# Kernel optimization log

Hardware: AMD Instinct MI355X
Metric: run time of the kernel (lower is better)

Reference implementation:

```python
import jax, jax.numpy as jnp
import numpy as np

B, S, HID = 16, 512, 2048
H = 4
D = HID // H  # 512; module requires S == D
SCALE = 1.0 / np.sqrt(D).astype(np.float32)


def setup_inputs() -> dict:
    key = jax.random.key(0)
    ks = jax.random.split(key, 6)
    std = 0.02
    inp = {"hidden_states": jax.random.normal(ks[0], (B, S, HID), jnp.float32)}
    names = ["q", "k", "v", "ck", "cv"]
    for i, n in enumerate(names):
        inp[f"W{n}"] = jax.random.normal(ks[i + 1], (HID, HID), jnp.float32) * std
        inp[f"b{n}"] = jnp.zeros((HID,), jnp.float32)
    return inp


def _heads(x):
    # [B,S,HID] -> [B,H,S,D]
    return x.reshape(B, S, H, D).transpose(0, 2, 1, 3)


def reference(hidden_states, Wq, bq, Wk, bk, Wv, bv, Wck, bck, Wcv, bcv):
    q = _heads(hidden_states @ Wq.T + bq)
    k = _heads(hidden_states @ Wk.T + bk)
    v = _heads(hidden_states @ Wv.T + bv)
    ck = _heads(hidden_states @ Wck.T + bck)
    cv = _heads(hidden_states @ Wcv.T + bcv)

    # scores1[b,h,q,j] = sum_d Q[b,h,q,d] K[b,h,j,d]
    s1 = jnp.einsum('bhqd,bhjd->bhqj', q, k)
    # scores2 = scores1 @ cube_key^T (valid since S == D)
    s2 = jnp.einsum('bhqj,bhmj->bhqm', s1, ck) * SCALE
    probs = jax.nn.softmax(s2, axis=-1)
    # ctx1 = probs @ V : [B,H,S,D]
    ctx = jnp.einsum('bhqm,bhmd->bhqd', probs, v)
    # ctx2 = ctx1 @ cube_value : [S,D]@[S,D] valid since S == D
    ctx = jnp.einsum('bhqm,bhme->bhqe', ctx, cv)
    # merge heads: [B,H,S,D] -> [B,S,HID]
    return ctx.transpose(0, 2, 1, 3).reshape(B, S, HID)
```

## Files before the change

### kernel.cpp

```cpp
#include <hip/hip_runtime.h>
#include <math.h>


typedef _Float16 f16;
typedef f16 f16x8 __attribute__((ext_vector_type(8)));
typedef float f32x4 __attribute__((ext_vector_type(4)));
typedef float f32x16 __attribute__((ext_vector_type(16)));

#define SB_STRIDE 520
#define QBLK 128
#define CHAIN_LDS (QBLK * SB_STRIDE * 2)
#define PROJ_LDS  131072

static constexpr float SCALE = 0.04419417382415922f;

__device__ __forceinline__ void gl_lds16(const f16* g, f16* l)
{
    __builtin_amdgcn_global_load_lds(
        (const __attribute__((address_space(1))) void*)g,
        (__attribute__((address_space(3))) void*)l, 16, 0, 0);
}

__global__ __launch_bounds__(256) void conv_f32_f16(const float* __restrict__ src,
                                                    f16* __restrict__ dst, int n)
{
    int i = (blockIdx.x * 256 + threadIdx.x) * 8;
    if (i + 8 <= n) {
        float4 a = *(const float4*)(src + i);
        float4 b = *(const float4*)(src + i + 4);
        f16 o[8] = {(f16)a.x, (f16)a.y, (f16)a.z, (f16)a.w,
                    (f16)b.x, (f16)b.y, (f16)b.z, (f16)b.w};
        *(int4*)(dst + i) = *(int4*)o;
    }
}

struct ProjPtrs {
    const f16* W[5];
    const float* bias[5];
    f16* dst[5];
};

__global__ __launch_bounds__(512, 2) void proj_f16(const f16* __restrict__ A, ProjPtrs P)
{
    extern __shared__ f16 sm[];
    const int z = blockIdx.z;
    const f16* __restrict__ W = P.W[z];
    const float* __restrict__ bias = P.bias[z];
    f16* __restrict__ dst = P.dst[z];
    const bool tr = (z == 2) || (z == 4);

    const int t    = threadIdx.x;
    const int lane = t & 63;
    const int wave = t >> 6;
    const int wr   = wave >> 2, wc = wave & 3;
    const int bm = blockIdx.y * 256, bn = blockIdx.x * 256;
    const int r16 = lane & 15;
    const int kq  = lane >> 4;

    const f16* gA = A + (size_t)(bm + (wave >> 1) * 16 + r16) * 2048 + ((wave & 1) * 4 + kq) * 8;
    const f16* gB = W + (size_t)(bn + (wave >> 1) * 16 + r16) * 2048 + ((wave & 1) * 4 + kq) * 8;
    const int stoff = wave * 512;

#define STG_A(c, h, tt)                                                     \
    {                                                                       \
        f16* d_ = sm + (c) * 32768 + (h) * 8192 + stoff;                    \
        gl_lds16(gA + (size_t)((h) * 128) * 2048 + (tt) * 64, d_);          \
        gl_lds16(gA + (size_t)((h) * 128 + 64) * 2048 + (tt) * 64, d_ + 4096); \
    }
#define STG_B(c, h, tt)                                                     \
    {                                                                       \
        f16* d_ = sm + (c) * 32768 + 16384 + (h) * 8192 + stoff;            \
        gl_lds16(gB + (size_t)((h) * 128) * 2048 + (tt) * 64, d_);          \
        gl_lds16(gB + (size_t)((h) * 128 + 64) * 2048 + (tt) * 64, d_ + 4096); \
    }

    f32x4 acc[8][4];
#pragma unroll
    for (int mf = 0; mf < 8; ++mf)
#pragma unroll
        for (int nf = 0; nf < 4; ++nf)
#pragma unroll
            for (int r = 0; r < 4; ++r) acc[mf][nf][r] = 0.f;

    STG_A(0, 0, 0); STG_A(0, 1, 0); STG_B(0, 0, 0); STG_B(0, 1, 0);
    STG_A(1, 0, 1); STG_A(1, 1, 1);
    asm volatile("s_waitcnt vmcnt(4)" ::: "memory");
    __builtin_amdgcn_s_barrier();
    asm volatile("" ::: "memory");

    const int aoff = kq * 128 + r16 * 8;

    f16x8 af[8][2], bf[4][2];

    for (int kt = 0; kt < 32; ++kt) {
        const int cur = kt & 1, nxt = cur ^ 1;
        const f16* pa = sm + cur * 32768 + wr * 8192 + aoff;
        const f16* pb = sm + cur * 32768 + 16384 + (wc >> 1) * 8192 + (wc & 1) * 4096 + aoff;

#pragma unroll
        for (int mf = 0; mf < 4; ++mf)
#pragma unroll
            for (int dk = 0; dk < 2; ++dk)
                af[mf][dk] = *(const f16x8*)(pa + mf * 1024 + dk * 512);
#pragma unroll
        for (int nf = 0; nf < 2; ++nf)
#pragma unroll
            for (int dk = 0; dk < 2; ++dk)
                bf[nf][dk] = *(const f16x8*)(pb + nf * 1024 + dk * 512);
        if (kt + 1 < 32) STG_B(nxt, 0, kt + 1);
        asm volatile("" ::: "memory");
        __builtin_amdgcn_s_barrier();
        asm volatile("s_waitcnt lgkmcnt(0)" ::: "memory");
        __builtin_amdgcn_sched_barrier(0);
        __builtin_amdgcn_s_setprio(1);
#pragma unroll
        for (int mf = 0; mf < 4; ++mf)
#pragma unroll
            for (int nf = 0; nf < 2; ++nf)
#pragma unroll
                for (int dk = 0; dk < 2; ++dk)
                    acc[mf][nf] = __builtin_amdgcn_mfma_f32_16x16x32_f16(
                        af[mf][dk], bf[nf][dk], acc[mf][nf], 0, 0, 0);
        __builtin_amdgcn_s_setprio(0);
        asm volatile("" ::: "memory");
        __builtin_amdgcn_s_barrier();
        asm volatile("" ::: "memory");

#pragma unroll
        for (int mf = 4; mf < 8; ++mf)
#pragma unroll
            for (int dk = 0; dk < 2; ++dk)
                af[mf][dk] = *(const f16x8*)(pa + mf * 1024 + dk * 512);
        if (kt + 1 < 32) STG_B(nxt, 1, kt + 1);
        asm volatile("" ::: "memory");
        __builtin_amdgcn_s_barrier();
        asm volatile("s_waitcnt lgkmcnt(0)" ::: "memory");
        __builtin_amdgcn_sched_barrier(0);
        __builtin_amdgcn_s_setprio(1);
#pragma unroll
        for (int mf = 4; mf < 8; ++mf)
#pragma unroll
            for (int nf = 0; nf < 2; ++nf)
#pragma unroll
                for (int dk = 0; dk < 2; ++dk)
                    acc[mf][nf] = __builtin_amdgcn_mfma_f32_16x16x32_f16(
                        af[mf][dk], bf[nf][dk], acc[mf][nf], 0, 0, 0);
        __builtin_amdgcn_s_setprio(0);
        asm volatile("" ::: "memory");
        __builtin_amdgcn_s_barrier();
        asm volatile("" ::: "memory");

#pragma unroll
        for (int nf = 2; nf < 4; ++nf)
#pragma unroll
            for (int dk = 0; dk < 2; ++dk)
                bf[nf][dk] = *(const f16x8*)(pb + nf * 1024 + dk * 512);
        if (kt + 2 < 32) STG_A(cur, 0, kt + 2);
        asm volatile("" ::: "memory");
        __builtin_amdgcn_s_barrier();
        asm volatile("s_waitcnt lgkmcnt(0)" ::: "memory");
        __builtin_amdgcn_sched_barrier(0);
        __builtin_amdgcn_s_setprio(1);
#pragma unroll
        for (int mf = 0; mf < 4; ++mf)
#pragma unroll
            for (int nf = 2; nf < 4; ++nf)
#pragma unroll
                for (int dk = 0; dk < 2; ++dk)
                    acc[mf][nf] = __builtin_amdgcn_mfma_f32_16x16x32_f16(
                        af[mf][dk], bf[nf][dk], acc[mf][nf], 0, 0, 0);
        __builtin_amdgcn_s_setprio(0);
        asm volatile("" ::: "memory");
        __builtin_amdgcn_s_barrier();
        asm volatile("" ::: "memory");

        if (kt + 2 < 32) STG_A(cur, 1, kt + 2);
        if (kt < 30) asm volatile("s_waitcnt vmcnt(4)" ::: "memory");
        else         asm volatile("s_waitcnt vmcnt(0)" ::: "memory");
        __builtin_amdgcn_s_barrier();
        asm volatile("" ::: "memory");
        __builtin_amdgcn_s_setprio(1);
#pragma unroll
        for (int mf = 4; mf < 8; ++mf)
#pragma unroll
            for (int nf = 2; nf < 4; ++nf)
#pragma unroll
                for (int dk = 0; dk < 2; ++dk)
                    acc[mf][nf] = __builtin_amdgcn_mfma_f32_16x16x32_f16(
                        af[mf][dk], bf[nf][dk], acc[mf][nf], 0, 0, 0);
        __builtin_amdgcn_s_setprio(0);
        asm volatile("" ::: "memory");
        __builtin_amdgcn_s_barrier();
        asm volatile("" ::: "memory");
    }
#undef STG_A
#undef STG_B

    const int wm = wr * 128, wn = wc * 64;
#pragma unroll
    for (int nf = 0; nf < 4; ++nf) {
        int n = bn + wn + nf * 16 + r16;
        float bb = bias[n];
        int h = n >> 9, d = n & 511;
#pragma unroll
        for (int mf = 0; mf < 8; ++mf) {
            int mbase = bm + wm + mf * 16 + (lane >> 4) * 4;
            int b = mbase >> 9, s0 = mbase & 511;
            if (!tr) {
#pragma unroll
                for (int r = 0; r < 4; ++r)
                    dst[(((size_t)(b * 4 + h)) * 512 + s0 + r) * 512 + d] =
                        (f16)(acc[mf][nf][r] + bb);
            } else {
                f16 pk[4];
#pragma unroll
                for (int r = 0; r < 4; ++r) pk[r] = (f16)(acc[mf][nf][r] + bb);
                *(float2*)(dst + (((size_t)(b * 4 + h)) * 512 + d) * 512 + s0) =
                    *(float2*)pk;
            }
        }
    }
}

__device__ __forceinline__ void stage_ntr(const f16* __restrict__ Bsrc,
                                          const f16* __restrict__ Sb,
                                          int t, f32x16 acc[4][2])
{
    const int lane = t & 63;
    const int wave = t >> 6;
    const int l31  = lane & 31;
    const int l5   = (lane >> 5) * 8;

#pragma unroll
    for (int mt = 0; mt < 4; ++mt)
#pragma unroll
        for (int nt = 0; nt < 2; ++nt)
#pragma unroll
            for (int r = 0; r < 16; ++r) acc[mt][nt][r] = 0.f;

    const f16* b0 = Bsrc + (size_t)(wave * 64 + l31) * 512 + l5;
    const f16* b1 = Bsrc + (size_t)(wave * 64 + 32 + l31) * 512 + l5;

    f16x8 bfA[2][2], bfB[2][2];

#define LDP(S, pp)                                              \
    do {                                                        \
        S[0][0] = *(const f16x8*)(b0 + (pp) * 32);              \
        S[0][1] = *(const f16x8*)(b0 + (pp) * 32 + 16);         \
        S[1][0] = *(const f16x8*)(b1 + (pp) * 32);              \
        S[1][1] = *(const f16x8*)(b1 + (pp) * 32 + 16);         \
    } while (0)

    LDP(bfA, 0);
    LDP(bfB, 1);

#pragma unroll
    for (int p = 0; p < 16; ++p) {
        f16x8 (&S)[2][2] = (p & 1) ? bfB : bfA;
#pragma unroll
        for (int dkh = 0; dkh < 2; ++dkh) {
            f16x8 af0 = *(const f16x8*)(Sb + (size_t)l31 * SB_STRIDE + p * 32 + dkh * 16 + l5);
            f16x8 af1 = *(const f16x8*)(Sb + (size_t)(32 + l31) * SB_STRIDE + p * 32 + dkh * 16 + l5);
            f16x8 af2 = *(const f16x8*)(Sb + (size_t)(64 + l31) * SB_STRIDE + p * 32 + dkh * 16 + l5);
            f16x8 af3 = *(const f16x8*)(Sb + (size_t)(96 + l31) * SB_STRIDE + p * 32 + dkh * 16 + l5);
            acc[0][0] = __builtin_amdgcn_mfma_f32_32x32x16_f16(af0, S[0][dkh], acc[0][0], 0, 0, 0);
            acc[0][1] = __builtin_amdgcn_mfma_f32_32x32x16_f16(af0, S[1][dkh], acc[0][1], 0, 0, 0);
            acc[1][0] = __builtin_amdgcn_mfma_f32_32x32x16_f16(af1, S[0][dkh], acc[1][0], 0, 0, 0);
            acc[1][1] = __builtin_amdgcn_mfma_f32_32x32x16_f16(af1, S[1][dkh], acc[1][1], 0, 0, 0);
            acc[2][0] = __builtin_amdgcn_mfma_f32_32x32x16_f16(af2, S[0][dkh], acc[2][0], 0, 0, 0);
            acc[2][1] = __builtin_amdgcn_mfma_f32_32x32x16_f16(af2, S[1][dkh], acc[2][1], 0, 0, 0);
            acc[3][0] = __builtin_amdgcn_mfma_f32_32x32x16_f16(af3, S[0][dkh], acc[3][0], 0, 0, 0);
            acc[3][1] = __builtin_amdgcn_mfma_f32_32x32x16_f16(af3, S[1][dkh], acc[3][1], 0, 0, 0);
        }
        if (p + 2 < 16) LDP(S, p + 2);
    }
#undef LDP
}

__device__ __forceinline__ void emit_to_S(f16* __restrict__ Sb, const f32x16 acc[4][2],
                                          int t, float scale)
{
    const int lane = t & 63;
    const int wn = (t >> 6) * 64;
#pragma unroll
    for (int mt = 0; mt < 4; ++mt)
#pragma unroll
        for (int nt = 0; nt < 2; ++nt) {
            int col = wn + nt * 32 + (lane & 31);
#pragma unroll
            for (int r = 0; r < 16; ++r) {
                int row = mt * 32 + (r & 3) + 8 * (r >> 2) + 4 * (lane >> 5);
                Sb[(size_t)row * SB_STRIDE + col] = (f16)(acc[mt][nt][r] * scale);
            }
        }
}

__global__ __launch_bounds__(512, 2) void chain_f16(
    const f16* __restrict__ q16, const f16* __restrict__ k16,
    const f16* __restrict__ ck16, const f16* __restrict__ vt16,
    const f16* __restrict__ cvt16, float* __restrict__ out,
    int bhmask, int q0shift)
{
    extern __shared__ f16 smem[];
    f16* Sb = smem;
    const int t = threadIdx.x;
    const int bh = blockIdx.x & bhmask;
    const int q0 = (blockIdx.x >> q0shift) * QBLK;
    const size_t SB = 512 * 512;

    const f16* Q = q16 + bh * SB;
    for (int i = t; i < 8192; i += 512) {
        int row = i >> 6, c = (i & 63) * 8;
        *(int4*)(Sb + (size_t)row * SB_STRIDE + c) =
            *(const int4*)(Q + (size_t)(q0 + row) * 512 + c);
    }
    __syncthreads();

    f32x16 acc[4][2];

    stage_ntr(k16 + bh * SB, Sb, t, acc);
    __syncthreads();
    emit_to_S(Sb, acc, t, 1.0f);
    __syncthreads();

    stage_ntr(ck16 + bh * SB, Sb, t, acc);
    __syncthreads();
    emit_to_S(Sb, acc, t, SCALE);
    __syncthreads();

    {
        const int lane = t & 63;
        const int wave = t >> 6;
        for (int rr = 0; rr < 16; ++rr) {
            int r = wave * 16 + rr;
            f16x8 xv = *(const f16x8*)(Sb + (size_t)r * SB_STRIDE + lane * 8);
            float x[8];
            float mx = -1e30f;
#pragma unroll
            for (int j = 0; j < 8; ++j) { x[j] = (float)xv[j]; mx = fmaxf(mx, x[j]); }
#pragma unroll
            for (int o = 32; o > 0; o >>= 1) mx = fmaxf(mx, __shfl_xor(mx, o));
            float s = 0.f;
#pragma unroll
            for (int j = 0; j < 8; ++j) { x[j] = __expf(x[j] - mx); s += x[j]; }
#pragma unroll
            for (int o = 32; o > 0; o >>= 1) s += __shfl_xor(s, o);
            float inv = 1.0f / s;
            f16x8 ov;
#pragma unroll
            for (int j = 0; j < 8; ++j) ov[j] = (f16)(x[j] * inv);
            *(f16x8*)(Sb + (size_t)r * SB_STRIDE + lane * 8) = ov;
        }
    }
    __syncthreads();

    stage_ntr(vt16 + bh * SB, Sb, t, acc);
    __syncthreads();
    emit_to_S(Sb, acc, t, 1.0f);
    __syncthreads();

    stage_ntr(cvt16 + bh * SB, Sb, t, acc);
    {
        const int lane = t & 63;
        const int wn = (t >> 6) * 64;
        int b = bh >> 2, h = bh & 3;
#pragma unroll
        for (int mt = 0; mt < 4; ++mt)
#pragma unroll
            for (int nt = 0; nt < 2; ++nt) {
                int col = h * 512 + wn + nt * 32 + (lane & 31);
#pragma unroll
                for (int r = 0; r < 16; ++r) {
                    int row = q0 + mt * 32 + (r & 3) + 8 * (r >> 2) + 4 * (lane >> 5);
                    out[((size_t)b * 512 + row) * 2048 + col] = acc[mt][nt][r];
                }
            }
    }
}

extern "C" void kernel_launch(void* const* d_in, const int* in_sizes, int n_in,
                              void* d_out, int out_size, void* d_ws, size_t ws_size,
                              hipStream_t stream)
{
    const float* hs = (const float*)d_in[0];
    const float* Wf[5] = {(const float*)d_in[1], (const float*)d_in[3],
                          (const float*)d_in[5], (const float*)d_in[7],
                          (const float*)d_in[9]};
    const float* bf[5] = {(const float*)d_in[2], (const float*)d_in[4],
                          (const float*)d_in[6], (const float*)d_in[8],
                          (const float*)d_in[10]};
    float* out = (float*)d_out;

    hipFuncSetAttribute((const void*)chain_f16,
                        hipFuncAttributeMaxDynamicSharedMemorySize, CHAIN_LDS);
    hipFuncSetAttribute((const void*)proj_f16,
                        hipFuncAttributeMaxDynamicSharedMemorySize, PROJ_LDS);

    f16* ws = (f16*)d_ws;
    const size_t WELEM = 2048ULL * 2048;
    const size_t FULLACT = 64ULL * 512 * 512;

    f16* W16[5];
    for (int i = 0; i < 5; ++i) W16[i] = ws + i * WELEM;
    f16* after_w = ws + 5 * WELEM;

    for (int i = 0; i < 5; ++i)
        conv_f32_f16<<<dim3(WELEM / 2048), 256, 0, stream>>>(Wf[i], W16[i], (int)WELEM);

    size_t full_need = (5 * WELEM + FULLACT + 5 * FULLACT) * sizeof(f16);
    if (ws_size >= full_need) {
        f16* hs16 = after_w;
        f16* act[5];
        for (int i = 0; i < 5; ++i) act[i] = after_w + FULLACT + i * FULLACT;

        conv_f32_f16<<<dim3(FULLACT / 2048), 256, 0, stream>>>(hs, hs16, (int)FULLACT);

        ProjPtrs P;
        for (int i = 0; i < 5; ++i) { P.W[i] = W16[i]; P.bias[i] = bf[i]; P.dst[i] = act[i]; }
        proj_f16<<<dim3(8, 32, 5), 512, PROJ_LDS, stream>>>(hs16, P);

        chain_f16<<<dim3(256), 512, CHAIN_LDS, stream>>>(
            act[0], act[1], act[3], act[2], act[4], out, 63, 6);
    } else {
        const size_t CHROW = 1048576ULL;
        const size_t CHACT = 4ULL * 512 * 512;
        f16* hs16c = after_w;
        f16* act[5];
        for (int i = 0; i < 5; ++i) act[i] = after_w + CHROW + i * CHACT;

        ProjPtrs P;
        for (int i = 0; i < 5; ++i) { P.W[i] = W16[i]; P.bias[i] = bf[i]; P.dst[i] = act[i]; }

        for (int c = 0; c < 16; ++c) {
            conv_f32_f16<<<dim3(CHROW / 2048), 256, 0, stream>>>(
                hs + c * CHROW, hs16c, (int)CHROW);
            proj_f16<<<dim3(8, 2, 5), 512, PROJ_LDS, stream>>>(hs16c, P);
            chain_f16<<<dim3(16), 512, CHAIN_LDS, stream>>>(
                act[0], act[1], act[3], act[2], act[4], out + c * CHROW, 3, 2);
        }
    }

    (void)in_sizes; (void)n_in; (void)out_size;
}
```

Baseline: 663.6 us.

## Double chain kernel to 16 waves with half the per-wave tile; swap proj grid order

The chain kernel now runs 1024 threads (16 waves), each computing a 128x32 output slice instead of 128x64. That halves the accumulator registers and B-fragment loads per wave and doubles the waves available to hide LDS and global latency. The softmax loop and Q staging are adjusted to match. Separately, the projection grid swaps the x/y block mapping so consecutive blocks walk the M dimension, which changes L2 reuse of weight tiles. The cost is that each A fragment read from LDS now feeds two fewer MFMAs per wave, raising total LDS traffic.

```diff
diff --git a/kernel.cpp b/kernel.cpp
--- a/kernel.cpp
+++ b/kernel.cpp
@@ -53,7 +53,7 @@
     const int lane = t & 63;
     const int wave = t >> 6;
     const int wr   = wave >> 2, wc = wave & 3;
-    const int bm = blockIdx.y * 256, bn = blockIdx.x * 256;
+    const int bm = blockIdx.x * 256, bn = blockIdx.y * 256;
     const int r16 = lane & 15;
     const int kq  = lane >> 4;
 
@@ -224,7 +224,7 @@
 
 __device__ __forceinline__ void stage_ntr(const f16* __restrict__ Bsrc,
                                           const f16* __restrict__ Sb,
-                                          int t, f32x16 acc[4][2])
+                                          int t, f32x16 acc[4])
 {
     const int lane = t & 63;
     const int wave = t >> 6;
@@ -234,21 +234,16 @@
 #pragma unroll
     for (int mt = 0; mt < 4; ++mt)
 #pragma unroll
-        for (int nt = 0; nt < 2; ++nt)
-#pragma unroll
-            for (int r = 0; r < 16; ++r) acc[mt][nt][r] = 0.f;
-
-    const f16* b0 = Bsrc + (size_t)(wave * 64 + l31) * 512 + l5;
-    const f16* b1 = Bsrc + (size_t)(wave * 64 + 32 + l31) * 512 + l5;
-
-    f16x8 bfA[2][2], bfB[2][2];
+        for (int r = 0; r < 16; ++r) acc[mt][r] = 0.f;
+
+    const f16* b0 = Bsrc + (size_t)(wave * 32 + l31) * 512 + l5;
+
+    f16x8 bfA[2], bfB[2];
 
 #define LDP(S, pp)                                              \
     do {                                                        \
-        S[0][0] = *(const f16x8*)(b0 + (pp) * 32);              \
-        S[0][1] = *(const f16x8*)(b0 + (pp) * 32 + 16);         \
-        S[1][0] = *(const f16x8*)(b1 + (pp) * 32);              \
-        S[1][1] = *(const f16x8*)(b1 + (pp) * 32 + 16);         \
+        S[0] = *(const f16x8*)(b0 + (pp) * 32);                 \
+        S[1] = *(const f16x8*)(b0 + (pp) * 32 + 16);            \
     } while (0)
 
     LDP(bfA, 0);
@@ -256,46 +251,40 @@
 
 #pragma unroll
     for (int p = 0; p < 16; ++p) {
-        f16x8 (&S)[2][2] = (p & 1) ? bfB : bfA;
+        f16x8 (&S)[2] = (p & 1) ? bfB : bfA;
 #pragma unroll
         for (int dkh = 0; dkh < 2; ++dkh) {
             f16x8 af0 = *(const f16x8*)(Sb + (size_t)l31 * SB_STRIDE + p * 32 + dkh * 16 + l5);
             f16x8 af1 = *(const f16x8*)(Sb + (size_t)(32 + l31) * SB_STRIDE + p * 32 + dkh * 16 + l5);
             f16x8 af2 = *(const f16x8*)(Sb + (size_t)(64 + l31) * SB_STRIDE + p * 32 + dkh * 16 + l5);
             f16x8 af3 = *(const f16x8*)(Sb + (size_t)(96 + l31) * SB_STRIDE + p * 32 + dkh * 16 + l5);
-            acc[0][0] = __builtin_amdgcn_mfma_f32_32x32x16_f16(af0, S[0][dkh], acc[0][0], 0, 0, 0);
-            acc[0][1] = __builtin_amdgcn_mfma_f32_32x32x16_f16(af0, S[1][dkh], acc[0][1], 0, 0, 0);
-            acc[1][0] = __builtin_amdgcn_mfma_f32_32x32x16_f16(af1, S[0][dkh], acc[1][0], 0, 0, 0);
-            acc[1][1] = __builtin_amdgcn_mfma_f32_32x32x16_f16(af1, S[1][dkh], acc[1][1], 0, 0, 0);
-            acc[2][0] = __builtin_amdgcn_mfma_f32_32x32x16_f16(af2, S[0][dkh], acc[2][0], 0, 0, 0);
-            acc[2][1] = __builtin_amdgcn_mfma_f32_32x32x16_f16(af2, S[1][dkh], acc[2][1], 0, 0, 0);
-            acc[3][0] = __builtin_amdgcn_mfma_f32_32x32x16_f16(af3, S[0][dkh], acc[3][0], 0, 0, 0);
-            acc[3][1] = __builtin_amdgcn_mfma_f32_32x32x16_f16(af3, S[1][dkh], acc[3][1], 0, 0, 0);
+            acc[0] = __builtin_amdgcn_mfma_f32_32x32x16_f16(af0, S[dkh], acc[0], 0, 0, 0);
+            acc[1] = __builtin_amdgcn_mfma_f32_32x32x16_f16(af1, S[dkh], acc[1], 0, 0, 0);
+            acc[2] = __builtin_amdgcn_mfma_f32_32x32x16_f16(af2, S[dkh], acc[2], 0, 0, 0);
+            acc[3] = __builtin_amdgcn_mfma_f32_32x32x16_f16(af3, S[dkh], acc[3], 0, 0, 0);
         }
         if (p + 2 < 16) LDP(S, p + 2);
     }
 #undef LDP
 }
 
-__device__ __forceinline__ void emit_to_S(f16* __restrict__ Sb, const f32x16 acc[4][2],
+__device__ __forceinline__ void emit_to_S(f16* __restrict__ Sb, const f32x16 acc[4],
                                           int t, float scale)
 {
     const int lane = t & 63;
-    const int wn = (t >> 6) * 64;
-#pragma unroll
-    for (int mt = 0; mt < 4; ++mt)
-#pragma unroll
-        for (int nt = 0; nt < 2; ++nt) {
-            int col = wn + nt * 32 + (lane & 31);
-#pragma unroll
-            for (int r = 0; r < 16; ++r) {
-                int row = mt * 32 + (r & 3) + 8 * (r >> 2) + 4 * (lane >> 5);
-                Sb[(size_t)row * SB_STRIDE + col] = (f16)(acc[mt][nt][r] * scale);
-            }
-        }
-}
-
-__global__ __launch_bounds__(512, 2) void chain_f16(
+    const int wn = (t >> 6) * 32;
+#pragma unroll
+    for (int mt = 0; mt < 4; ++mt) {
+        int col = wn + (lane & 31);
+#pragma unroll
+        for (int r = 0; r < 16; ++r) {
+            int row = mt * 32 + (r & 3) + 8 * (r >> 2) + 4 * (lane >> 5);
+            Sb[(size_t)row * SB_STRIDE + col] = (f16)(acc[mt][r] * scale);
+        }
+    }
+}
+
+__global__ __launch_bounds__(1024, 4) void chain_f16(
     const f16* __restrict__ q16, const f16* __restrict__ k16,
     const f16* __restrict__ ck16, const f16* __restrict__ vt16,
     const f16* __restrict__ cvt16, float* __restrict__ out,
@@ -309,14 +298,14 @@
     const size_t SB = 512 * 512;
 
     const f16* Q = q16 + bh * SB;
-    for (int i = t; i < 8192; i += 512) {
+    for (int i = t; i < 8192; i += 1024) {
         int row = i >> 6, c = (i & 63) * 8;
         *(int4*)(Sb + (size_t)row * SB_STRIDE + c) =
             *(const int4*)(Q + (size_t)(q0 + row) * 512 + c);
     }
     __syncthreads();
 
-    f32x16 acc[4][2];
+    f32x16 acc[4];
 
     stage_ntr(k16 + bh * SB, Sb, t, acc);
     __syncthreads();
@@ -331,8 +320,8 @@
     {
         const int lane = t & 63;
         const int wave = t >> 6;
-        for (int rr = 0; rr < 16; ++rr) {
-            int r = wave * 16 + rr;
+        for (int rr = 0; rr < 8; ++rr) {
+            int r = wave * 8 + rr;
             f16x8 xv = *(const f16x8*)(Sb + (size_t)r * SB_STRIDE + lane * 8);
             float x[8];
             float mx = -1e30f;
@@ -362,19 +351,17 @@
     stage_ntr(cvt16 + bh * SB, Sb, t, acc);
     {
         const int lane = t & 63;
-        const int wn = (t >> 6) * 64;
+        const int wn = (t >> 6) * 32;
         int b = bh >> 2, h = bh & 3;
 #pragma unroll
-        for (int mt = 0; mt < 4; ++mt)
-#pragma unroll
-            for (int nt = 0; nt < 2; ++nt) {
-                int col = h * 512 + wn + nt * 32 + (lane & 31);
-#pragma unroll
-                for (int r = 0; r < 16; ++r) {
-                    int row = q0 + mt * 32 + (r & 3) + 8 * (r >> 2) + 4 * (lane >> 5);
-                    out[((size_t)b * 512 + row) * 2048 + col] = acc[mt][nt][r];
-                }
+        for (int mt = 0; mt < 4; ++mt) {
+            int col = h * 512 + wn + (lane & 31);
+#pragma unroll
+            for (int r = 0; r < 16; ++r) {
+                int row = q0 + mt * 32 + (r & 3) + 8 * (r >> 2) + 4 * (lane >> 5);
+                out[((size_t)b * 512 + row) * 2048 + col] = acc[mt][r];
             }
+        }
     }
 }
 
@@ -417,9 +404,9 @@
 
         ProjPtrs P;
         for (int i = 0; i < 5; ++i) { P.W[i] = W16[i]; P.bias[i] = bf[i]; P.dst[i] = act[i]; }
-        proj_f16<<<dim3(8, 32, 5), 512, PROJ_LDS, stream>>>(hs16, P);
-
-        chain_f16<<<dim3(256), 512, CHAIN_LDS, stream>>>(
+        proj_f16<<<dim3(32, 8, 5), 512, PROJ_LDS, stream>>>(hs16, P);
+
+        chain_f16<<<dim3(256), 1024, CHAIN_LDS, stream>>>(
             act[0], act[1], act[3], act[2], act[4], out, 63, 6);
     } else {
         const size_t CHROW = 1048576ULL;
@@ -434,8 +421,8 @@
         for (int c = 0; c < 16; ++c) {
             conv_f32_f16<<<dim3(CHROW / 2048), 256, 0, stream>>>(
                 hs + c * CHROW, hs16c, (int)CHROW);
-            proj_f16<<<dim3(8, 2, 5), 512, PROJ_LDS, stream>>>(hs16c, P);
-            chain_f16<<<dim3(16), 512, CHAIN_LDS, stream>>>(
+            proj_f16<<<dim3(2, 8, 5), 512, PROJ_LDS, stream>>>(hs16c, P);
+            chain_f16<<<dim3(16), 1024, CHAIN_LDS, stream>>>(
                 act[0], act[1], act[3], act[2], act[4], out + c * CHROW, 3, 2);
         }
     }
```

After: 670.6 us. Within noise of the previous version (+1.1%).
